# Kernel optimization log

Measured on AMD Instinct MI355X. Metric: run time of the kernel, lower is better.

## Reference

```python
import jax, jax.numpy as jnp
import numpy as np

LN_EPS = 1e-5

def setup_inputs() -> dict:
    key = jax.random.key(0)
    ks = jax.random.split(key, 10)
    B, L, D2 = 64, 512, 16  # batch, max_len_text, 2*n_degree
    V, D, C = 8000, 256, 4  # n_word, d_model, n_category
    E = (V - 1) * V + 1      # edge-weight table size
    x = jax.random.randint(ks[0], (B, L), 0, V, dtype=jnp.int32)
    nb_x = jax.random.randint(ks[1], (B, L, D2), 0, V, dtype=jnp.int32)
    w_edge = jax.random.randint(ks[2], (B, L, D2), 0, E, dtype=jnp.int32)
    emb_weight = jax.random.normal(ks[3], (V, D), jnp.float32) * 0.02
    emb_weight = emb_weight.at[0].set(0.0)  # padding_idx=0
    w_edge_table = jax.random.normal(ks[4], (E, 1), jnp.float32) * 0.02
    w_edge_table = w_edge_table.at[0].set(0.0)
    eta_table = jax.random.normal(ks[5], (V, 1), jnp.float32) * 0.02
    eta_table = eta_table.at[0].set(0.0)
    ln_gamma = jnp.ones((D,), jnp.float32)
    ln_beta = jnp.zeros((D,), jnp.float32)
    fc_w = jax.random.normal(ks[6], (D, C), jnp.float32) * 0.02
    fc_b = jnp.zeros((C,), jnp.float32)
    return {"x": x, "nb_x": nb_x, "w_edge": w_edge,
            "emb_weight": emb_weight, "w_edge_table": w_edge_table,
            "eta_table": eta_table, "ln_gamma": ln_gamma, "ln_beta": ln_beta,
            "fc_w": fc_w, "fc_b": fc_b}

def _layernorm(h, gamma, beta):
    mu = jnp.mean(h, axis=-1, keepdims=True)
    var = jnp.mean(jnp.square(h - mu), axis=-1, keepdims=True)
    return (h - mu) * jax.lax.rsqrt(var + LN_EPS) * gamma + beta

def reference(x, nb_x, w_edge, emb_weight, w_edge_table, eta_table,
              ln_gamma, ln_beta, fc_w, fc_b):
    # idx_nodes: (B, L, 2*deg + 1) -- neighbors then self
    idx_nodes = jnp.concatenate([nb_x, x[..., None]], axis=-1)
    emb_nodes = emb_weight[idx_nodes]                  # (B, L, 2d+1, D)
    emb_nodes = _layernorm(emb_nodes, ln_gamma, ln_beta)
    we = w_edge_table[w_edge]                          # (B, L, 2d, 1)
    msg_nb = jnp.max(we * emb_nodes[:, :, :-1, :], axis=2)  # (B, L, D)
    eta = eta_table[x]                                 # (B, L, 1)
    h_node = (1.0 - eta) * msg_nb + eta * emb_nodes[:, :, -1, :]
    scores = h_node.sum(axis=1) @ fc_w + fc_b          # (B, C)
    return scores
```

## Files before the change

### kernel.cpp

```cpp
#include <hip/hip_runtime.h>
#include <math.h>

#define DV   256
#define BB   64
#define LL   512
#define DEG2 16
#define VV   8000
#define CC   4
#define LPW  4
#define NW   4
#define NLC  32
#define NSL  2
#define NE   (BB*LL*DEG2)
#define LN_EPS 1e-5f

typedef _Float16 half4 __attribute__((ext_vector_type(4)));
typedef _Float16 half8 __attribute__((ext_vector_type(8)));
typedef float    f32x2 __attribute__((ext_vector_type(2)));
typedef float    f32x4 __attribute__((ext_vector_type(4)));
typedef int      i32x4 __attribute__((ext_vector_type(4)));

__device__ __forceinline__ half8 sxor_h8(half8 v, int mask) {
    i32x4 i = __builtin_bit_cast(i32x4, v);
    i32x4 s;
    #pragma unroll
    for (int k = 0; k < 4; ++k) s[k] = __shfl_xor(i[k], mask);
    return __builtin_bit_cast(half8, s);
}

__global__ void __launch_bounds__(64) ln_rows_kernel(
    const float* __restrict__ emb, const float* __restrict__ gamma,
    const float* __restrict__ beta,
    const int* __restrict__ w_edge, const float* __restrict__ we_table,
    half4* __restrict__ out, float* __restrict__ we_flat)
{
    const int row = blockIdx.x;
    const int ln  = threadIdx.x;

    for (int g = blockIdx.x * 64 + ln; g < NE; g += VV * 64)
        we_flat[g] = we_table[w_edge[g]];

    const f32x4 v = ((const f32x4*)(emb + row * DV))[ln];

    float s = v[0] + v[1] + v[2] + v[3];
    #pragma unroll
    for (int off = 32; off > 0; off >>= 1) s += __shfl_xor(s, off);
    const float mu = s * (1.0f / DV);

    f32x4 c;
    #pragma unroll
    for (int k = 0; k < 4; ++k) c[k] = v[k] - mu;

    float q = c[0]*c[0] + c[1]*c[1] + c[2]*c[2] + c[3]*c[3];
    #pragma unroll
    for (int off = 32; off > 0; off >>= 1) q += __shfl_xor(q, off);
    const float rs = rsqrtf(q * (1.0f / DV) + LN_EPS);

    const f32x4 g  = ((const f32x4*)gamma)[ln];
    const f32x4 bt = ((const f32x4*)beta)[ln];

    half4 h;
    #pragma unroll
    for (int k = 0; k < 4; ++k) h[k] = (_Float16)(c[k] * rs * g[k] + bt[k]);

    const int sl = ln >> 5;
    const int cc = ln & 31;
    ((half4*)out)[((size_t)sl * VV + row) * 32 + cc] = h;
}

__global__ void __launch_bounds__(256) gnn_kernel(
    const int*   __restrict__ nb_x,
    const int*   __restrict__ x,
    const float* __restrict__ we_flat,
    const float* __restrict__ eta_table,
    const half8* __restrict__ norm_emb,
    float*       __restrict__ h_part)
{
    const int blk = blockIdx.x;
    const int xcd = blk & 7;
    const int u   = blk >> 3;
    const int sl  = xcd >> 2;
    const int qq  = (xcd & 3) + (u << 2);
    const int b   = qq >> 5;
    const int lc  = qq & 31;

    const int tid = threadIdx.x;
    const int w   = tid >> 6;
    const int ln  = tid & 63;
    const int q   = ln >> 4;
    const int c8  = ln & 15;

    const int l0   = lc * 16 + w * LPW;
    const int base = b * LL + l0;
    const size_t sRow = (size_t)sl * VV;

    const int   nbv = __builtin_nontemporal_load(nb_x    + base * DEG2 + ln);
    const float wev = __builtin_nontemporal_load(we_flat + base * DEG2 + ln);

    int xv = 0; float etv = 0.0f;
    if (ln < LPW) { xv = x[base + ln]; etv = eta_table[xv]; }

    const int   srow = __shfl(xv, q);
    const half8 se   = norm_emb[(sRow + srow) * 16 + c8];
    const float eta  = __shfl(etv, q);
    const float om   = 1.0f - eta;

    float acc[8] = {0,0,0,0,0,0,0,0};

    #pragma unroll
    for (int li = 0; li < LPW; ++li) {
        half8 m;
        #pragma unroll
        for (int k = 0; k < 8; ++k) m[k] = (_Float16)(-65504.0f);

        #pragma unroll
        for (int k4 = 0; k4 < 4; ++k4) {
            const int   jsrc = li * DEG2 + k4 * 4 + q;
            const int   idx  = __shfl(nbv, jsrc);
            const float wj   = __shfl(wev, jsrc);
            half8 w8;
            #pragma unroll
            for (int t = 0; t < 8; ++t) w8[t] = (_Float16)wj;
            const half8 e = norm_emb[(sRow + idx) * 16 + c8];
            m = __builtin_elementwise_max(m, w8 * e);
        }
        m = __builtin_elementwise_max(m, sxor_h8(m, 16));
        m = __builtin_elementwise_max(m, sxor_h8(m, 32));

        if (q == li) {
            #pragma unroll
            for (int k = 0; k < 8; ++k)
                acc[k] += om * (float)m[k] + eta * (float)se[k];
        }
    }

    #pragma unroll
    for (int k = 0; k < 8; ++k) {
        acc[k] += __shfl_xor(acc[k], 16);
        acc[k] += __shfl_xor(acc[k], 32);
    }

    __shared__ float s_acc[NW][DV / NSL];
    if (ln < 16) {
        f32x4 a0 = {acc[0], acc[1], acc[2], acc[3]};
        f32x4 a1 = {acc[4], acc[5], acc[6], acc[7]};
        ((f32x4*)&s_acc[w][c8 * 8])[0] = a0;
        ((f32x4*)&s_acc[w][c8 * 8])[1] = a1;
    }
    __syncthreads();
    if (w == 0) {
        const int d2 = ln * 2;
        f32x2 r;
        r[0] = s_acc[0][d2]     + s_acc[1][d2]     + s_acc[2][d2]     + s_acc[3][d2];
        r[1] = s_acc[0][d2 + 1] + s_acc[1][d2 + 1] + s_acc[2][d2 + 1] + s_acc[3][d2 + 1];
        __builtin_nontemporal_store(r,
            (f32x2*)(h_part + (size_t)(b * NLC + lc) * DV + sl * (DV / NSL)) + ln);
    }
}

__global__ void __launch_bounds__(256) fc_kernel(
    const float* __restrict__ h_part,
    const float* __restrict__ fc_w,
    const float* __restrict__ fc_b,
    float*       __restrict__ out)
{
    const int b  = blockIdx.x;
    const int d  = threadIdx.x;
    const int w  = d >> 6;
    const int ln = d & 63;

    float h = 0.0f;
    #pragma unroll 8
    for (int lc = 0; lc < NLC; ++lc)
        h += h_part[(size_t)(b * NLC + lc) * DV + d];

    float p[CC];
    #pragma unroll
    for (int c = 0; c < CC; ++c) p[c] = h * fc_w[d * CC + c];

    #pragma unroll
    for (int c = 0; c < CC; ++c)
        #pragma unroll
        for (int off = 32; off > 0; off >>= 1) p[c] += __shfl_xor(p[c], off);

    __shared__ float s_red[NW][CC];
    if (ln == 0) {
        #pragma unroll
        for (int c = 0; c < CC; ++c) s_red[w][c] = p[c];
    }
    __syncthreads();
    if (d < CC)
        out[b * CC + d] = s_red[0][d] + s_red[1][d] + s_red[2][d] + s_red[3][d] + fc_b[d];
}

extern "C" void kernel_launch(void* const* d_in, const int* in_sizes, int n_in,
                              void* d_out, int out_size, void* d_ws, size_t ws_size,
                              hipStream_t stream) {
    const int*   x        = (const int*)  d_in[0];
    const int*   nb_x     = (const int*)  d_in[1];
    const int*   w_edge   = (const int*)  d_in[2];
    const float* emb_w    = (const float*)d_in[3];
    const float* we_table = (const float*)d_in[4];
    const float* eta_tab  = (const float*)d_in[5];
    const float* ln_gamma = (const float*)d_in[6];
    const float* ln_beta  = (const float*)d_in[7];
    const float* fc_w     = (const float*)d_in[8];
    const float* fc_b     = (const float*)d_in[9];
    float* out = (float*)d_out;

    char* ws = (char*)d_ws;
    half4* norm_emb = (half4*)(ws);
    float* we_flat  = (float*)(ws + 4096000);
    float* h_part   = (float*)(ws + 4096000 + 2097152);

    ln_rows_kernel<<<VV, 64, 0, stream>>>(emb_w, ln_gamma, ln_beta,
                                          w_edge, we_table, norm_emb, we_flat);

    gnn_kernel<<<BB * NLC * NSL, 256, 0, stream>>>(
        nb_x, x, we_flat, eta_tab, (const half8*)norm_emb, h_part);

    fc_kernel<<<BB, 256, 0, stream>>>(h_part, fc_w, fc_b, out);
}
```

Measured before the change: 43.11 us.

## Use persistent work-stealing blocks with XCC-aware slice assignment in GNN kernel

Replaces the fixed block-to-work mapping (which assumed round-robin XCD dispatch) with a persistent loop where each block atomically grabs work items from a per-slice counter chosen by the hardware XCC id, falling back to the other slice when exhausted. This aims to keep each embedding half-table resident in the L2 of the XCDs that use it and to balance load dynamically. It adds a memset launch, per-item atomics, and extra barriers per iteration.

Result: slower. 127.3 us (+195.2%).

```diff
diff --git a/kernel.cpp b/kernel.cpp
--- a/kernel.cpp
+++ b/kernel.cpp
@@ -11,6 +11,7 @@
 #define NW   4
 #define NLC  32
 #define NSL  2
+#define NITEMS (BB*NLC)
 #define NE   (BB*LL*DEG2)
 #define LN_EPS 1e-5f
 
@@ -68,21 +69,18 @@
     ((half4*)out)[((size_t)sl * VV + row) * 32 + cc] = h;
 }
 
-__global__ void __launch_bounds__(256) gnn_kernel(
+__global__ void __launch_bounds__(256) gnn_ws_kernel(
     const int*   __restrict__ nb_x,
     const int*   __restrict__ x,
     const float* __restrict__ we_flat,
     const float* __restrict__ eta_table,
     const half8* __restrict__ norm_emb,
-    float*       __restrict__ h_part)
+    float*       __restrict__ h_part,
+    int*         __restrict__ counters)
 {
-    const int blk = blockIdx.x;
-    const int xcd = blk & 7;
-    const int u   = blk >> 3;
-    const int sl  = xcd >> 2;
-    const int qq  = (xcd & 3) + (u << 2);
-    const int b   = qq >> 5;
-    const int lc  = qq & 31;
+    int xcc;
+    asm volatile("s_getreg_b32 %0, hwreg(HW_REG_XCC_ID)" : "=s"(xcc));
+    const int myslice = (xcc >> 2) & 1;
 
     const int tid = threadIdx.x;
     const int w   = tid >> 6;
@@ -90,71 +88,93 @@
     const int q   = ln >> 4;
     const int c8  = ln & 15;
 
-    const int l0   = lc * 16 + w * LPW;
-    const int base = b * LL + l0;
-    const size_t sRow = (size_t)sl * VV;
-
-    const int   nbv = __builtin_nontemporal_load(nb_x    + base * DEG2 + ln);
-    const float wev = __builtin_nontemporal_load(we_flat + base * DEG2 + ln);
-
-    int xv = 0; float etv = 0.0f;
-    if (ln < LPW) { xv = x[base + ln]; etv = eta_table[xv]; }
-
-    const int   srow = __shfl(xv, q);
-    const half8 se   = norm_emb[(sRow + srow) * 16 + c8];
-    const float eta  = __shfl(etv, q);
-    const float om   = 1.0f - eta;
-
-    float acc[8] = {0,0,0,0,0,0,0,0};
-
-    #pragma unroll
-    for (int li = 0; li < LPW; ++li) {
-        half8 m;
-        #pragma unroll
-        for (int k = 0; k < 8; ++k) m[k] = (_Float16)(-65504.0f);
-
-        #pragma unroll
-        for (int k4 = 0; k4 < 4; ++k4) {
-            const int   jsrc = li * DEG2 + k4 * 4 + q;
-            const int   idx  = __shfl(nbv, jsrc);
-            const float wj   = __shfl(wev, jsrc);
-            half8 w8;
+    __shared__ int s_widx, s_slice;
+    __shared__ float s_acc[NW][DV / NSL];
+
+    for (;;) {
+        __syncthreads();
+        if (tid == 0) {
+            int v = atomicAdd(&counters[myslice], 1);
+            int s = myslice;
+            if (v >= NITEMS) {
+                v = atomicAdd(&counters[1 - myslice], 1);
+                s = 1 - myslice;
+            }
+            s_widx = v; s_slice = s;
+        }
+        __syncthreads();
+        const int widx = s_widx;
+        const int sl   = s_slice;
+        if (widx >= NITEMS) return;
+
+        const int b  = widx >> 5;
+        const int lc = widx & 31;
+
+        const int l0   = lc * 16 + w * LPW;
+        const int base = b * LL + l0;
+        const size_t sRow = (size_t)sl * VV;
+
+        const int   nbv = __builtin_nontemporal_load(nb_x    + base * DEG2 + ln);
+        const float wev = __builtin_nontemporal_load(we_flat + base * DEG2 + ln);
+
+        int xv = 0; float etv = 0.0f;
+        if (ln < LPW) { xv = x[base + ln]; etv = eta_table[xv]; }
+
+        const int   srow = __shfl(xv, q);
+        const half8 se   = norm_emb[(sRow + srow) * 16 + c8];
+        const float eta  = __shfl(etv, q);
+        const float om   = 1.0f - eta;
+
+        float acc[8] = {0,0,0,0,0,0,0,0};
+
+        #pragma unroll
+        for (int li = 0; li < LPW; ++li) {
+            half8 m;
             #pragma unroll
-            for (int t = 0; t < 8; ++t) w8[t] = (_Float16)wj;
-            const half8 e = norm_emb[(sRow + idx) * 16 + c8];
-            m = __builtin_elementwise_max(m, w8 * e);
-        }
-        m = __builtin_elementwise_max(m, sxor_h8(m, 16));
-        m = __builtin_elementwise_max(m, sxor_h8(m, 32));
-
-        if (q == li) {
+            for (int k = 0; k < 8; ++k) m[k] = (_Float16)(-65504.0f);
+
             #pragma unroll
-            for (int k = 0; k < 8; ++k)
-                acc[k] += om * (float)m[k] + eta * (float)se[k];
-        }
-    }
-
-    #pragma unroll
-    for (int k = 0; k < 8; ++k) {
-        acc[k] += __shfl_xor(acc[k], 16);
-        acc[k] += __shfl_xor(acc[k], 32);
-    }
-
-    __shared__ float s_acc[NW][DV / NSL];
-    if (ln < 16) {
-        f32x4 a0 = {acc[0], acc[1], acc[2], acc[3]};
-        f32x4 a1 = {acc[4], acc[5], acc[6], acc[7]};
-        ((f32x4*)&s_acc[w][c8 * 8])[0] = a0;
-        ((f32x4*)&s_acc[w][c8 * 8])[1] = a1;
-    }
-    __syncthreads();
-    if (w == 0) {
-        const int d2 = ln * 2;
-        f32x2 r;
-        r[0] = s_acc[0][d2]     + s_acc[1][d2]     + s_acc[2][d2]     + s_acc[3][d2];
-        r[1] = s_acc[0][d2 + 1] + s_acc[1][d2 + 1] + s_acc[2][d2 + 1] + s_acc[3][d2 + 1];
-        __builtin_nontemporal_store(r,
-            (f32x2*)(h_part + (size_t)(b * NLC + lc) * DV + sl * (DV / NSL)) + ln);
+            for (int k4 = 0; k4 < 4; ++k4) {
+                const int   jsrc = li * DEG2 + k4 * 4 + q;
+                const int   idx  = __shfl(nbv, jsrc);
+                const float wj   = __shfl(wev, jsrc);
+                half8 w8;
+                #pragma unroll
+                for (int t = 0; t < 8; ++t) w8[t] = (_Float16)wj;
+                const half8 e = norm_emb[(sRow + idx) * 16 + c8];
+                m = __builtin_elementwise_max(m, w8 * e);
+            }
+            m = __builtin_elementwise_max(m, sxor_h8(m, 16));
+            m = __builtin_elementwise_max(m, sxor_h8(m, 32));
+
+            if (q == li) {
+                #pragma unroll
+                for (int k = 0; k < 8; ++k)
+                    acc[k] += om * (float)m[k] + eta * (float)se[k];
+            }
+        }
+
+        #pragma unroll
+        for (int k = 0; k < 8; ++k) {
+            acc[k] += __shfl_xor(acc[k], 16);
+            acc[k] += __shfl_xor(acc[k], 32);
+        }
+
+        if (ln < 16) {
+            f32x4 a0 = {acc[0], acc[1], acc[2], acc[3]};
+            f32x4 a1 = {acc[4], acc[5], acc[6], acc[7]};
+            ((f32x4*)&s_acc[w][c8 * 8])[0] = a0;
+            ((f32x4*)&s_acc[w][c8 * 8])[1] = a1;
+        }
+        __syncthreads();
+        if (w == 0) {
+            const int d2 = ln * 2;
+            f32x2 r;
+            r[0] = s_acc[0][d2]     + s_acc[1][d2]     + s_acc[2][d2]     + s_acc[3][d2];
+            r[1] = s_acc[0][d2 + 1] + s_acc[1][d2 + 1] + s_acc[2][d2 + 1] + s_acc[3][d2 + 1];
+            __builtin_nontemporal_store(r,
+                (f32x2*)(h_part + (size_t)(b * NLC + lc) * DV + sl * (DV / NSL)) + ln);
+        }
     }
 }
 
@@ -212,12 +232,15 @@
     half4* norm_emb = (half4*)(ws);
     float* we_flat  = (float*)(ws + 4096000);
     float* h_part   = (float*)(ws + 4096000 + 2097152);
+    int*   counters = (int*)  (ws + 4096000 + 2097152 + 2097152);
+
+    hipMemsetAsync(counters, 0, 2 * sizeof(int), stream);
 
     ln_rows_kernel<<<VV, 64, 0, stream>>>(emb_w, ln_gamma, ln_beta,
                                           w_edge, we_table, norm_emb, we_flat);
 
-    gnn_kernel<<<BB * NLC * NSL, 256, 0, stream>>>(
-        nb_x, x, we_flat, eta_tab, (const half8*)norm_emb, h_part);
+    gnn_ws_kernel<<<2048, 256, 0, stream>>>(
+        nb_x, x, we_flat, eta_tab, (const half8*)norm_emb, h_part, counters);
 
     fc_kernel<<<BB, 256, 0, stream>>>(h_part, fc_w, fc_b, out);
 }
```
